# Kernel optimization log

Measured on AMD Instinct MI355X. Metric: run time of the kernel, lower is better.

## Reference

```python
import jax, jax.numpy as jnp
import numpy as np
import math

B, S, F, H, E = 2, 1024, 512, 2048, 8
EPS = 1e-10

def setup_inputs() -> dict:
    key = jax.random.key(0)
    ks = jax.random.split(key, 6)
    s1 = math.sqrt(1.0 / (F + H))  # complex_xavier_init std for F->H
    s2 = math.sqrt(1.0 / (H + F))  # std for H->F
    return {
        'x_r': jax.random.normal(ks[0], (B, S, F), jnp.float32),
        'x_i': jax.random.normal(ks[1], (B, S, F), jnp.float32),
        'Wr1': jax.random.normal(ks[2], (E, F, H), jnp.float32) * s1,
        'Wi1': jax.random.normal(ks[3], (E, F, H), jnp.float32) * s1,
        'br1': jnp.zeros((E, H), jnp.float32),
        'bi1': jnp.zeros((E, H), jnp.float32),
        'mb': jnp.zeros((E, H), jnp.float32),  # ModReLU bias
        'Wr2': jax.random.normal(ks[4], (E, H, F), jnp.float32) * s2,
        'Wi2': jax.random.normal(ks[5], (E, H, F), jnp.float32) * s2,
        'br2': jnp.zeros((E, F), jnp.float32),
        'bi2': jnp.zeros((E, F), jnp.float32),
    }

def reference(x_r, x_i, Wr1, Wi1, br1, bi1, mb, Wr2, Wi2, br2, bi2):
    n_exp = Wr1.shape[0]
    # --- PhaseRouter: deterministic top-1 routing by mean token phase ---
    phase = jnp.arctan2(x_i, x_r)                      # angle(x), (B,S,F)
    mean_cos = jnp.mean(jnp.cos(phase), axis=-1)
    mean_sin = jnp.mean(jnp.sin(phase), axis=-1)
    token_phase = jnp.arctan2(mean_sin, mean_cos)      # (B,S)
    norm_phase = (token_phase + jnp.pi) / (2 * jnp.pi)
    idx = jnp.clip(jnp.floor(norm_phase * n_exp).astype(jnp.int32), 0, n_exp - 1)
    probs = jax.nn.one_hot(idx, n_exp, dtype=x_r.dtype)  # (B,S,E)
    # --- dense all-expert complex MLP (as in source: every expert on every token) ---
    # layer 1: complex linear F->H, per expert
    h_r = (jnp.einsum('bsf,efh->ebsh', x_r, Wr1) - jnp.einsum('bsf,efh->ebsh', x_i, Wi1)
           + br1[:, None, None, :])
    h_i = (jnp.einsum('bsf,efh->ebsh', x_r, Wi1) + jnp.einsum('bsf,efh->ebsh', x_i, Wr1)
           + bi1[:, None, None, :])
    # ModReLU: relu(|z|+b) * z/(|z|+eps)
    amp = jnp.sqrt(h_r * h_r + h_i * h_i + EPS)
    scale = jax.nn.relu(amp + mb[:, None, None, :]) / (amp + EPS)
    h_r = scale * h_r
    h_i = scale * h_i
    # layer 2: complex linear H->F, per expert
    y_r = (jnp.einsum('ebsh,ehf->ebsf', h_r, Wr2) - jnp.einsum('ebsh,ehf->ebsf', h_i, Wi2)
           + br2[:, None, None, :])
    y_i = (jnp.einsum('ebsh,ehf->ebsf', h_r, Wi2) + jnp.einsum('ebsh,ehf->ebsf', h_i, Wr2)
           + bi2[:, None, None, :])
    # combine: expert_weight * mask == probs * probs (one-hot, 0/1)
    w = probs * probs                                   # (B,S,E)
    out_r = jnp.einsum('ebsf,bse->bsf', y_r, w)
    out_i = jnp.einsum('ebsf,bse->bsf', y_i, w)
    return jnp.stack([out_r, out_i])                    # (2,B,S,F): real, imag
```

## Files before the change

kernel.cpp:

```cpp
#include <hip/hip_runtime.h>
#include <hip/hip_bf16.h>

#define TOKENS 2048
#define FDIM 512
#define HDIM 2048
#define NEXP 8
#define PI_F 3.14159265358979323846f

typedef __attribute__((ext_vector_type(8))) short bf16x8;
typedef __attribute__((ext_vector_type(4))) float f32x4;

__device__ __forceinline__ unsigned short f2bf(float f) {
  unsigned int u = __float_as_uint(f);
  unsigned int r = (u + 0x7fffu + ((u >> 16) & 1u)) >> 16;
  return (unsigned short)r;
}

__device__ __forceinline__ void gload16(const void* g, void* l) {
  __builtin_amdgcn_global_load_lds(
      (const __attribute__((address_space(1))) unsigned int*)g,
      (__attribute__((address_space(3))) unsigned int*)l, 16, 0, 0);
}

__global__ __launch_bounds__(256) void route_kernel(
    const float* __restrict__ xr, const float* __restrict__ xi,
    int* __restrict__ idx, int* __restrict__ counts)
{
  int tid = threadIdx.x;
  int t = blockIdx.x * 8 + (tid >> 5);
  int l = tid & 31;
  const float* r  = xr + (size_t)t * FDIM;
  const float* im = xi + (size_t)t * FDIM;
  float sc = 0.f, ss = 0.f;
  #pragma unroll
  for (int p = 0; p < 4; ++p) {
    int f = p * 128 + l * 4;
    float4 a4 = *(const float4*)(r + f);
    float4 b4 = *(const float4*)(im + f);
    float av[4] = {a4.x, a4.y, a4.z, a4.w};
    float bv[4] = {b4.x, b4.y, b4.z, b4.w};
    #pragma unroll
    for (int j = 0; j < 4; ++j) {
      float h2 = av[j] * av[j] + bv[j] * bv[j];
      if (h2 > 0.f) {
        float rs = rsqrtf(h2);
        sc += av[j] * rs;
        ss += bv[j] * rs;
      } else {
        sc += 1.f;
      }
    }
  }
  #pragma unroll
  for (int off = 16; off > 0; off >>= 1) {
    sc += __shfl_down(sc, off, 32);
    ss += __shfl_down(ss, off, 32);
  }
  if (l == 0) {
    float phase = atan2f(ss, sc);
    float norm = (phase + PI_F) / (2.f * PI_F);
    int e = (int)floorf(norm * (float)NEXP);
    e = min(max(e, 0), NEXP - 1);
    idx[t] = e;
    atomicAdd(&counts[e], 1);
  }
}

__global__ __launch_bounds__(256) void scatter_kernel(
    const int* __restrict__ idx, const int* __restrict__ counts,
    int* __restrict__ offs, int* __restrict__ perm, int* __restrict__ rexp)
{
  __shared__ int base_e[NEXP];
  __shared__ int tcnt[256][NEXP];
  int tid = threadIdx.x;
  if (tid == 0) {
    int acc = 0;
    for (int e = 0; e < NEXP; ++e) { base_e[e] = acc; offs[e] = acc; acc += counts[e]; }
  }
  int t0 = tid * 8;
  int eo[8];
  int loc[NEXP];
  #pragma unroll
  for (int e = 0; e < NEXP; ++e) loc[e] = 0;
  #pragma unroll
  for (int j = 0; j < 8; ++j) { eo[j] = idx[t0 + j]; loc[eo[j]]++; }
  #pragma unroll
  for (int e = 0; e < NEXP; ++e) tcnt[tid][e] = loc[e];
  __syncthreads();
  if (tid < NEXP) {
    int e = tid, run = 0;
    for (int i = 0; i < 256; ++i) { int v = tcnt[i][e]; tcnt[i][e] = run; run += v; }
  }
  __syncthreads();
  #pragma unroll
  for (int e = 0; e < NEXP; ++e) loc[e] = base_e[e] + tcnt[tid][e];
  #pragma unroll
  for (int j = 0; j < 8; ++j) {
    int e = eo[j];
    int pos = loc[e]++;
    perm[pos] = t0 + j;
    rexp[pos] = e;
  }
}

__global__ __launch_bounds__(256) void pack_x_kernel(
    const float* __restrict__ xr, const float* __restrict__ xi,
    const int* __restrict__ perm,
    short* __restrict__ Ar, short* __restrict__ Ai)
{
  int gid = blockIdx.x * 256 + threadIdx.x;
  int i = gid >> 7;
  int c4 = (gid & 127) * 4;
  int tok = perm[i];
  float4 r = *(const float4*)(xr + (size_t)tok * FDIM + c4);
  float4 m = *(const float4*)(xi + (size_t)tok * FDIM + c4);
  unsigned short orr[4] = { f2bf(r.x), f2bf(r.y), f2bf(r.z), f2bf(r.w) };
  unsigned short oii[4] = { f2bf(m.x), f2bf(m.y), f2bf(m.z), f2bf(m.w) };
  *(int2*)(Ar + (size_t)i * FDIM + c4) = *(const int2*)orr;
  *(int2*)(Ai + (size_t)i * FDIM + c4) = *(const int2*)oii;
}

template<int K, int N>
__global__ __launch_bounds__(256) void pack_w_kernel(
    const float* __restrict__ Wr, const float* __restrict__ Wi,
    short* __restrict__ Wp)
{
  int e = blockIdx.z;
  int k0 = blockIdx.y * 32, n0 = blockIdx.x * 32;
  __shared__ float tr[32][33], ti[32][33];
  int tid = threadIdx.x;
  int row = tid >> 3, c4 = (tid & 7) * 4;
  const float* wr = Wr + ((size_t)e * K + k0) * N + n0;
  const float* wi = Wi + ((size_t)e * K + k0) * N + n0;
  float4 vr = *(const float4*)(wr + (size_t)row * N + c4);
  float4 vi = *(const float4*)(wi + (size_t)row * N + c4);
  *(float4*)&tr[row][c4] = vr;
  *(float4*)&ti[row][c4] = vi;
  __syncthreads();
  int nl = tid >> 3, k4 = (tid & 7) * 4;
  unsigned short pr[4], pi[4];
  #pragma unroll
  for (int j = 0; j < 4; ++j) {
    pr[j] = f2bf(tr[k4 + j][nl]);
    pi[j] = f2bf(ti[k4 + j][nl]);
  }
  size_t b0 = (((size_t)e * 2 + 0) * N + n0 + nl) * K + k0 + k4;
  size_t b1 = (((size_t)e * 2 + 1) * N + n0 + nl) * K + k0 + k4;
  *(int2*)(Wp + b0) = *(const int2*)pr;
  *(int2*)(Wp + b1) = *(const int2*)pi;
}

template<int LDK, int NC, int NX, bool IS_L1>
__global__ __launch_bounds__(256) void gemm_cplx(
    const short* __restrict__ Apr, const short* __restrict__ Api,
    const short* __restrict__ Wp,
    const int* __restrict__ counts, const int* __restrict__ offs,
    const float* __restrict__ bre, const float* __restrict__ bim,
    const float* __restrict__ mb,
    short* __restrict__ Or, short* __restrict__ Oi,
    unsigned int* __restrict__ P)
{
  constexpr int KT = 16;
  int bid = blockIdx.x;
  int virt = (bid & 7) * 256 + (bid >> 3);
  int e = virt >> 8, rem = virt & 255;
  int x = rem % NX;
  int q = rem / NX;
  int y = q & 7, s = q >> 3;
  int cnt = counts[e];
  int row0 = y * 64;
  if (row0 >= cnt) return;
  int base = offs[e];
  int n0c = x * 64;
  int kbase = s * 512;

  __shared__ __align__(16) short As[3][2][64][32];
  __shared__ __align__(16) short Ws[3][2][64][32];

  int tid = threadIdx.x;
  int lane = tid & 63;
  int w = tid >> 6, wm = w >> 1, wn = w & 1;
  int lr = lane & 15, g = lane >> 4;
  int ssw = g ^ ((lr >> 1) & 3);

  int srl = tid >> 2, slt = tid & 3;
  int sc = (slt ^ ((srl >> 1) & 3)) * 16;
  int arow = min(row0 + srl, cnt - 1);
  const char* pAr = (const char*)(Apr + (size_t)(base + arow) * LDK + kbase) + sc;
  const char* pAi = (const char*)(Api + (size_t)(base + arow) * LDK + kbase) + sc;
  const short* We = Wp + (size_t)e * 2 * NC * LDK;
  const char* pW0 = (const char*)(We + (size_t)(n0c + srl) * LDK + kbase) + sc;
  const char* pW1 = (const char*)(We + ((size_t)NC + n0c + srl) * LDK + kbase) + sc;

  auto STAGE = [&](int buf, int t) {
    char* ab = (char*)&As[0][0][0][0] + buf * 8192;
    gload16(pAr + t * 64, ab + tid * 16);
    gload16(pAi + t * 64, ab + 4096 + tid * 16);
    char* wb = (char*)&Ws[0][0][0][0] + buf * 8192;
    gload16(pW0 + t * 64, wb + tid * 16);
    gload16(pW1 + t * 64, wb + 4096 + tid * 16);
  };

  f32x4 accr[2][2], acci[2][2];
  #pragma unroll
  for (int m = 0; m < 2; ++m)
    #pragma unroll
    for (int n = 0; n < 2; ++n) { accr[m][n] = 0.f; acci[m][n] = 0.f; }

  const bf16x8 SGN = {(short)0x8000, (short)0x8000, (short)0x8000, (short)0x8000,
                      (short)0x8000, (short)0x8000, (short)0x8000, (short)0x8000};

  auto COMPUTE = [&](int buf) {
    const short* Ab = &As[0][0][0][0] + buf * 4096;
    const short* Wb = &Ws[0][0][0][0] + buf * 4096;
    bf16x8 ar[2], ai[2], wr[2], wi[2], wni[2];
    #pragma unroll
    for (int m = 0; m < 2; ++m) {
      int off = (wm * 32 + m * 16 + lr) * 32 + ssw * 8;
      ar[m] = *(const bf16x8*)(Ab + off);
      ai[m] = *(const bf16x8*)(Ab + 2048 + off);
    }
    #pragma unroll
    for (int n = 0; n < 2; ++n) {
      int offw = (wn * 32 + n * 16 + lr) * 32 + ssw * 8;
      wr[n] = *(const bf16x8*)(Wb + offw);
      wi[n] = *(const bf16x8*)(Wb + 2048 + offw);
      wni[n] = wi[n] ^ SGN;
    }
    #pragma unroll
    for (int m = 0; m < 2; ++m)
      #pragma unroll
      for (int n = 0; n < 2; ++n) {
        accr[m][n] = __builtin_amdgcn_mfma_f32_16x16x32_bf16(ar[m], wr[n],  accr[m][n], 0, 0, 0);
        accr[m][n] = __builtin_amdgcn_mfma_f32_16x16x32_bf16(ai[m], wni[n], accr[m][n], 0, 0, 0);
        acci[m][n] = __builtin_amdgcn_mfma_f32_16x16x32_bf16(ar[m], wi[n],  acci[m][n], 0, 0, 0);
        acci[m][n] = __builtin_amdgcn_mfma_f32_16x16x32_bf16(ai[m], wr[n],  acci[m][n], 0, 0, 0);
      }
  };

  STAGE(0, 0);
  STAGE(1, 1);
  for (int t = 0; t < KT; ++t) {
    if (t < KT - 1) asm volatile("s_waitcnt vmcnt(4)" ::: "memory");
    else            asm volatile("s_waitcnt vmcnt(0)" ::: "memory");
    __builtin_amdgcn_s_barrier();
    if (t + 2 < KT) STAGE((t + 2) % 3, t + 2);
    COMPUTE(t % 3);
  }

  #pragma unroll
  for (int m = 0; m < 2; ++m) {
    #pragma unroll
    for (int qq = 0; qq < 4; ++qq) {
      int row = row0 + wm * 32 + m * 16 + g * 4 + qq;
      if (row >= cnt) continue;
      #pragma unroll
      for (int n = 0; n < 2; ++n) {
        int c = n0c + wn * 32 + n * 16 + lr;
        if constexpr (IS_L1) {
          float hr = accr[m][n][qq] + bre[e * NC + c];
          float hi = acci[m][n][qq] + bim[e * NC + c];
          float s2 = hr * hr + hi * hi + 1e-10f;
          float rr = __frsqrt_rn(s2);
          float amp = s2 * rr;
          float scl = fmaxf(amp + mb[e * NC + c], 0.f) * rr;
          Or[(size_t)(base + row) * NC + c] = (short)f2bf(hr * scl);
          Oi[(size_t)(base + row) * NC + c] = (short)f2bf(hi * scl);
        } else {
          unsigned pv = (unsigned)f2bf(accr[m][n][qq])
                      | ((unsigned)f2bf(acci[m][n][qq]) << 16);
          P[((size_t)s * TOKENS + base + row) * 512 + c] = pv;
        }
      }
    }
  }
}

__global__ __launch_bounds__(256) void finalize_kernel(
    const unsigned int* __restrict__ P, const float* __restrict__ br2,
    const float* __restrict__ bi2, const int* __restrict__ perm,
    const int* __restrict__ rexp, float* __restrict__ out)
{
  int gid = blockIdx.x * 256 + threadIdx.x;
  int i = gid >> 7;
  int c4 = (gid & 127) * 4;
  float sr[4] = {0.f, 0.f, 0.f, 0.f}, si[4] = {0.f, 0.f, 0.f, 0.f};
  #pragma unroll
  for (int s = 0; s < 4; ++s) {
    uint4 u = *(const uint4*)(P + ((size_t)s * TOKENS + i) * 512 + c4);
    unsigned uv[4] = {u.x, u.y, u.z, u.w};
    #pragma unroll
    for (int j = 0; j < 4; ++j) {
      sr[j] += __uint_as_float(uv[j] << 16);
      si[j] += __uint_as_float(uv[j] & 0xFFFF0000u);
    }
  }
  int e = rexp[i], tok = perm[i];
  float4 br = *(const float4*)(br2 + e * FDIM + c4);
  float4 bi = *(const float4*)(bi2 + e * FDIM + c4);
  float4 vr = {sr[0] + br.x, sr[1] + br.y, sr[2] + br.z, sr[3] + br.w};
  float4 vi = {si[0] + bi.x, si[1] + bi.y, si[2] + bi.z, si[3] + bi.w};
  *(float4*)(out + (size_t)tok * FDIM + c4) = vr;
  *(float4*)(out + (size_t)TOKENS * FDIM + (size_t)tok * FDIM + c4) = vi;
}

extern "C" void kernel_launch(void* const* d_in, const int* in_sizes, int n_in,
                              void* d_out, int out_size, void* d_ws, size_t ws_size,
                              hipStream_t stream)
{
  const float* xr  = (const float*)d_in[0];
  const float* xi  = (const float*)d_in[1];
  const float* Wr1 = (const float*)d_in[2];
  const float* Wi1 = (const float*)d_in[3];
  const float* br1 = (const float*)d_in[4];
  const float* bi1 = (const float*)d_in[5];
  const float* mb  = (const float*)d_in[6];
  const float* Wr2 = (const float*)d_in[7];
  const float* Wi2 = (const float*)d_in[8];
  const float* br2 = (const float*)d_in[9];
  const float* bi2 = (const float*)d_in[10];
  float* out = (float*)d_out;

  char* ws = (char*)d_ws;
  int* counts = (int*)(ws + 0);
  int* offs   = (int*)(ws + 64);
  int* idx    = (int*)(ws + 128);
  int* perm   = (int*)(ws + 8320);
  int* rexp   = (int*)(ws + 16512);

  size_t off = 32768;
  short* A1r = (short*)(ws + off); off += (size_t)TOKENS * FDIM * 2;
  short* A1i = (short*)(ws + off); off += (size_t)TOKENS * FDIM * 2;
  short* A2r = (short*)(ws + off); off += (size_t)TOKENS * HDIM * 2;
  short* A2i = (short*)(ws + off); off += (size_t)TOKENS * HDIM * 2;
  short* W1p = (short*)(ws + off); off += (size_t)NEXP * 2 * HDIM * FDIM * 2;
  short* W2p = (short*)(ws + off); off += (size_t)NEXP * 2 * FDIM * HDIM * 2;
  unsigned int* P = (unsigned int*)(ws + off);

  hipMemsetAsync(counts, 0, 64, stream);
  route_kernel<<<TOKENS / 8, 256, 0, stream>>>(xr, xi, idx, counts);
  scatter_kernel<<<1, 256, 0, stream>>>(idx, counts, offs, perm, rexp);

  pack_x_kernel<<<TOKENS * 128 / 256, 256, 0, stream>>>(xr, xi, perm, A1r, A1i);
  pack_w_kernel<FDIM, HDIM><<<dim3(HDIM / 32, FDIM / 32, NEXP), 256, 0, stream>>>(
      Wr1, Wi1, W1p);
  pack_w_kernel<HDIM, FDIM><<<dim3(FDIM / 32, HDIM / 32, NEXP), 256, 0, stream>>>(
      Wr2, Wi2, W2p);

  gemm_cplx<FDIM, HDIM, 32, true><<<2048, 256, 0, stream>>>(
      A1r, A1i, W1p, counts, offs, br1, bi1, mb, A2r, A2i, nullptr);
  gemm_cplx<HDIM, FDIM, 8, false><<<2048, 256, 0, stream>>>(
      A2r, A2i, W2p, counts, offs, nullptr, nullptr, nullptr, nullptr, nullptr, P);

  finalize_kernel<<<TOKENS * 128 / 256, 256, 0, stream>>>(
      P, br2, bi2, perm, rexp, out);
}
```

Before: 129.9 us.

## Fuse routing with weight packing and switch GEMM to double-buffered LDS

Routing and both weight-packing passes now run in one launch: the first 256 blocks compute token routing and the remaining blocks transpose and convert weights to bf16. This removes two kernel launches and lets the small routing work overlap with the bandwidth-heavy weight packing. The complex GEMM also drops from three LDS stages to two, issuing the next prefetch after compute behind an extra barrier. That cuts shared memory per block, which may allow more blocks per CU, but adds one synchronisation per K step.

Result: faster. 123.1 us (-5.2%).

```diff
diff --git a/kernel.cpp b/kernel.cpp
--- a/kernel.cpp
+++ b/kernel.cpp
@@ -22,112 +22,15 @@
       (__attribute__((address_space(3))) unsigned int*)l, 16, 0, 0);
 }
 
-__global__ __launch_bounds__(256) void route_kernel(
-    const float* __restrict__ xr, const float* __restrict__ xi,
-    int* __restrict__ idx, int* __restrict__ counts)
-{
-  int tid = threadIdx.x;
-  int t = blockIdx.x * 8 + (tid >> 5);
-  int l = tid & 31;
-  const float* r  = xr + (size_t)t * FDIM;
-  const float* im = xi + (size_t)t * FDIM;
-  float sc = 0.f, ss = 0.f;
-  #pragma unroll
-  for (int p = 0; p < 4; ++p) {
-    int f = p * 128 + l * 4;
-    float4 a4 = *(const float4*)(r + f);
-    float4 b4 = *(const float4*)(im + f);
-    float av[4] = {a4.x, a4.y, a4.z, a4.w};
-    float bv[4] = {b4.x, b4.y, b4.z, b4.w};
-    #pragma unroll
-    for (int j = 0; j < 4; ++j) {
-      float h2 = av[j] * av[j] + bv[j] * bv[j];
-      if (h2 > 0.f) {
-        float rs = rsqrtf(h2);
-        sc += av[j] * rs;
-        ss += bv[j] * rs;
-      } else {
-        sc += 1.f;
-      }
-    }
-  }
-  #pragma unroll
-  for (int off = 16; off > 0; off >>= 1) {
-    sc += __shfl_down(sc, off, 32);
-    ss += __shfl_down(ss, off, 32);
-  }
-  if (l == 0) {
-    float phase = atan2f(ss, sc);
-    float norm = (phase + PI_F) / (2.f * PI_F);
-    int e = (int)floorf(norm * (float)NEXP);
-    e = min(max(e, 0), NEXP - 1);
-    idx[t] = e;
-    atomicAdd(&counts[e], 1);
-  }
-}
-
-__global__ __launch_bounds__(256) void scatter_kernel(
-    const int* __restrict__ idx, const int* __restrict__ counts,
-    int* __restrict__ offs, int* __restrict__ perm, int* __restrict__ rexp)
-{
-  __shared__ int base_e[NEXP];
-  __shared__ int tcnt[256][NEXP];
-  int tid = threadIdx.x;
-  if (tid == 0) {
-    int acc = 0;
-    for (int e = 0; e < NEXP; ++e) { base_e[e] = acc; offs[e] = acc; acc += counts[e]; }
-  }
-  int t0 = tid * 8;
-  int eo[8];
-  int loc[NEXP];
-  #pragma unroll
-  for (int e = 0; e < NEXP; ++e) loc[e] = 0;
-  #pragma unroll
-  for (int j = 0; j < 8; ++j) { eo[j] = idx[t0 + j]; loc[eo[j]]++; }
-  #pragma unroll
-  for (int e = 0; e < NEXP; ++e) tcnt[tid][e] = loc[e];
-  __syncthreads();
-  if (tid < NEXP) {
-    int e = tid, run = 0;
-    for (int i = 0; i < 256; ++i) { int v = tcnt[i][e]; tcnt[i][e] = run; run += v; }
-  }
-  __syncthreads();
-  #pragma unroll
-  for (int e = 0; e < NEXP; ++e) loc[e] = base_e[e] + tcnt[tid][e];
-  #pragma unroll
-  for (int j = 0; j < 8; ++j) {
-    int e = eo[j];
-    int pos = loc[e]++;
-    perm[pos] = t0 + j;
-    rexp[pos] = e;
-  }
-}
-
-__global__ __launch_bounds__(256) void pack_x_kernel(
-    const float* __restrict__ xr, const float* __restrict__ xi,
-    const int* __restrict__ perm,
-    short* __restrict__ Ar, short* __restrict__ Ai)
-{
-  int gid = blockIdx.x * 256 + threadIdx.x;
-  int i = gid >> 7;
-  int c4 = (gid & 127) * 4;
-  int tok = perm[i];
-  float4 r = *(const float4*)(xr + (size_t)tok * FDIM + c4);
-  float4 m = *(const float4*)(xi + (size_t)tok * FDIM + c4);
-  unsigned short orr[4] = { f2bf(r.x), f2bf(r.y), f2bf(r.z), f2bf(r.w) };
-  unsigned short oii[4] = { f2bf(m.x), f2bf(m.y), f2bf(m.z), f2bf(m.w) };
-  *(int2*)(Ar + (size_t)i * FDIM + c4) = *(const int2*)orr;
-  *(int2*)(Ai + (size_t)i * FDIM + c4) = *(const int2*)oii;
-}
-
 template<int K, int N>
-__global__ __launch_bounds__(256) void pack_w_kernel(
+__device__ __forceinline__ void pack_w_body(
     const float* __restrict__ Wr, const float* __restrict__ Wi,
-    short* __restrict__ Wp)
-{
-  int e = blockIdx.z;
-  int k0 = blockIdx.y * 32, n0 = blockIdx.x * 32;
-  __shared__ float tr[32][33], ti[32][33];
+    short* __restrict__ Wp, int b, float (*tr)[33], float (*ti)[33])
+{
+  int per_e = (K / 32) * (N / 32);
+  int e = b / per_e;
+  int rem = b % per_e;
+  int k0 = (rem / (N / 32)) * 32, n0 = (rem % (N / 32)) * 32;
   int tid = threadIdx.x;
   int row = tid >> 3, c4 = (tid & 7) * 4;
   const float* wr = Wr + ((size_t)e * K + k0) * N + n0;
@@ -148,6 +51,115 @@
   size_t b1 = (((size_t)e * 2 + 1) * N + n0 + nl) * K + k0 + k4;
   *(int2*)(Wp + b0) = *(const int2*)pr;
   *(int2*)(Wp + b1) = *(const int2*)pi;
+}
+
+__global__ __launch_bounds__(256) void route_packw_kernel(
+    const float* __restrict__ xr, const float* __restrict__ xi,
+    int* __restrict__ idx, int* __restrict__ counts,
+    const float* __restrict__ Wr1, const float* __restrict__ Wi1,
+    const float* __restrict__ Wr2, const float* __restrict__ Wi2,
+    short* __restrict__ W1p, short* __restrict__ W2p)
+{
+  __shared__ float tr[32][33], ti[32][33];
+  int bid = blockIdx.x;
+  if (bid < 256) {
+    int tid = threadIdx.x;
+    int t = bid * 8 + (tid >> 5);
+    int l = tid & 31;
+    const float* r  = xr + (size_t)t * FDIM;
+    const float* im = xi + (size_t)t * FDIM;
+    float sc = 0.f, ss = 0.f;
+    #pragma unroll
+    for (int p = 0; p < 4; ++p) {
+      int f = p * 128 + l * 4;
+      float4 a4 = *(const float4*)(r + f);
+      float4 b4 = *(const float4*)(im + f);
+      float av[4] = {a4.x, a4.y, a4.z, a4.w};
+      float bv[4] = {b4.x, b4.y, b4.z, b4.w};
+      #pragma unroll
+      for (int j = 0; j < 4; ++j) {
+        float h2 = av[j] * av[j] + bv[j] * bv[j];
+        if (h2 > 0.f) {
+          float rs = rsqrtf(h2);
+          sc += av[j] * rs;
+          ss += bv[j] * rs;
+        } else {
+          sc += 1.f;
+        }
+      }
+    }
+    #pragma unroll
+    for (int off = 16; off > 0; off >>= 1) {
+      sc += __shfl_down(sc, off, 32);
+      ss += __shfl_down(ss, off, 32);
+    }
+    if (l == 0) {
+      float phase = atan2f(ss, sc);
+      float norm = (phase + PI_F) / (2.f * PI_F);
+      int e = (int)floorf(norm * (float)NEXP);
+      e = min(max(e, 0), NEXP - 1);
+      idx[t] = e;
+      atomicAdd(&counts[e], 1);
+    }
+  } else {
+    int b = bid - 256;
+    if (b < 8192) pack_w_body<FDIM, HDIM>(Wr1, Wi1, W1p, b, tr, ti);
+    else          pack_w_body<HDIM, FDIM>(Wr2, Wi2, W2p, b - 8192, tr, ti);
+  }
+}
+
+__global__ __launch_bounds__(256) void scatter_kernel(
+    const int* __restrict__ idx, const int* __restrict__ counts,
+    int* __restrict__ offs, int* __restrict__ perm, int* __restrict__ rexp)
+{
+  __shared__ int base_e[NEXP];
+  __shared__ int tcnt[256][NEXP];
+  int tid = threadIdx.x;
+  if (tid == 0) {
+    int acc = 0;
+    for (int e = 0; e < NEXP; ++e) { base_e[e] = acc; offs[e] = acc; acc += counts[e]; }
+  }
+  int t0 = tid * 8;
+  int eo[8];
+  int loc[NEXP];
+  #pragma unroll
+  for (int e = 0; e < NEXP; ++e) loc[e] = 0;
+  #pragma unroll
+  for (int j = 0; j < 8; ++j) { eo[j] = idx[t0 + j]; loc[eo[j]]++; }
+  #pragma unroll
+  for (int e = 0; e < NEXP; ++e) tcnt[tid][e] = loc[e];
+  __syncthreads();
+  if (tid < NEXP) {
+    int e = tid, run = 0;
+    for (int i = 0; i < 256; ++i) { int v = tcnt[i][e]; tcnt[i][e] = run; run += v; }
+  }
+  __syncthreads();
+  #pragma unroll
+  for (int e = 0; e < NEXP; ++e) loc[e] = base_e[e] + tcnt[tid][e];
+  #pragma unroll
+  for (int j = 0; j < 8; ++j) {
+    int e = eo[j];
+    int pos = loc[e]++;
+    perm[pos] = t0 + j;
+    rexp[pos] = e;
+  }
+}
+
+__global__ __launch_bounds__(256) void pack_x_kernel(
+    const float* __restrict__ xr, const float* __restrict__ xi,
+    const int* __restrict__ perm,
+    short* __restrict__ Ar, short* __restrict__ Ai)
+{
+  int gid = blockIdx.x * 256 + threadIdx.x;
+  int i = gid >> 7;
+  int c4 = (gid & 127) * 4;
+  int tok = perm[i];
+  float4 r = *(const float4*)(xr + (size_t)tok * FDIM + c4);
+  float4 m = *(const float4*)(xi + (size_t)tok * FDIM + c4);
+  unsigned short orr[4] = { f2bf(r.x), f2bf(r.y), f2bf(r.z), f2bf(r.w) };
+  unsigned short oii[4] = { f2bf(m.x), f2bf(m.y), f2bf(m.z), f2bf(m.w) };
+  *(int2*)(Ar + (size_t)i * FDIM + c4) = *(const int2*)orr;
+  *(int2*)(Ai + (size_t)i * FDIM + c4) = *(const int2*)oii;
 }
 
 template<int LDK, int NC, int NX, bool IS_L1>
@@ -174,8 +186,8 @@
   int n0c = x * 64;
   int kbase = s * 512;
 
-  __shared__ __align__(16) short As[3][2][64][32];
-  __shared__ __align__(16) short Ws[3][2][64][32];
+  __shared__ __align__(16) short As[2][2][64][32];
+  __shared__ __align__(16) short Ws[2][2][64][32];
 
   int tid = threadIdx.x;
   int lane = tid & 63;
@@ -244,8 +256,9 @@
     if (t < KT - 1) asm volatile("s_waitcnt vmcnt(4)" ::: "memory");
     else            asm volatile("s_waitcnt vmcnt(0)" ::: "memory");
     __builtin_amdgcn_s_barrier();
-    if (t + 2 < KT) STAGE((t + 2) % 3, t + 2);
-    COMPUTE(t % 3);
+    COMPUTE(t & 1);
+    __builtin_amdgcn_s_barrier();
+    if (t + 2 < KT) STAGE(t & 1, t + 2);
   }
 
   #pragma unroll
@@ -338,14 +351,10 @@
   unsigned int* P = (unsigned int*)(ws + off);
 
   hipMemsetAsync(counts, 0, 64, stream);
-  route_kernel<<<TOKENS / 8, 256, 0, stream>>>(xr, xi, idx, counts);
+  route_packw_kernel<<<256 + 16384, 256, 0, stream>>>(
+      xr, xi, idx, counts, Wr1, Wi1, Wr2, Wi2, W1p, W2p);
   scatter_kernel<<<1, 256, 0, stream>>>(idx, counts, offs, perm, rexp);
-
   pack_x_kernel<<<TOKENS * 128 / 256, 256, 0, stream>>>(xr, xi, perm, A1r, A1i);
-  pack_w_kernel<FDIM, HDIM><<<dim3(HDIM / 32, FDIM / 32, NEXP), 256, 0, stream>>>(
-      Wr1, Wi1, W1p);
-  pack_w_kernel<HDIM, FDIM><<<dim3(FDIM / 32, HDIM / 32, NEXP), 256, 0, stream>>>(
-      Wr2, Wi2, W2p);
 
   gemm_cplx<FDIM, HDIM, 32, true><<<2048, 256, 0, stream>>>(
       A1r, A1i, W1p, counts, offs, br1, bi1, mb, A2r, A2i, nullptr);
```
